# Kernel tuning notes

Measured on AMD Instinct MI355X. Metric: run time of the kernel, lower is better.

Reference implementation:

```python
import jax, jax.numpy as jnp
import numpy as np
from jax import lax

TEMP = 65.0
CLIP_DIST = 0.01
EPS = 1e-6  # torch PairwiseDistance eps (added to the difference) and log eps
NTOKEN, NINP, NHID = 32000, 1024, 1024
SEQ_LEN, BSZ, NSAMPLES = 128, 64, 10


def setup_inputs() -> dict:
    key = jax.random.key(0)
    ks = jax.random.split(key, 7)
    data = jax.random.randint(ks[0], (SEQ_LEN, BSZ), 0, NTOKEN)
    samples = jax.random.randint(ks[1], (NSAMPLES, SEQ_LEN * BSZ), 0, NTOKEN)
    # encoder init_weights: uniform(-0.1, 0.1); RNN weights small to avoid tanh saturation
    emb_W = jax.random.uniform(ks[2], (NTOKEN, NINP), minval=-0.1, maxval=0.1, dtype=jnp.float32)
    W_ih = jax.random.normal(ks[3], (NHID, NINP), dtype=jnp.float32) * 0.03
    b_ih = jax.random.normal(ks[4], (NHID,), dtype=jnp.float32) * 0.01
    W_hh = jax.random.normal(ks[5], (NHID, NHID), dtype=jnp.float32) * 0.03
    b_hh = jax.random.normal(ks[6], (NHID,), dtype=jnp.float32) * 0.01
    return {"data": data, "samples": samples, "emb_W": emb_W,
            "W_ih": W_ih, "b_ih": b_ih, "W_hh": W_hh, "b_hh": b_hh}


def _sq_pdist(x, y):
    # torch PairwiseDistance(p=2).pow(2): ||x - y + eps||^2 (no sqrt needed)
    d = x - y + EPS
    return jnp.sum(d * d, axis=-1)


def reference(data, samples, emb_W, W_ih, b_ih, W_hh, b_hh):
    seq_len, bsz = data.shape
    nhid = W_hh.shape[0]
    emb = emb_W[data]                                  # [S, B, ninp]
    h0 = jnp.zeros((bsz, nhid), dtype=emb_W.dtype)

    def step(h, e):
        h_new = jnp.tanh(e @ W_ih.T + b_ih + h @ W_hh.T + b_hh)
        return h_new, h_new

    _, outs = lax.scan(step, h0, emb)                  # [S, B, H]
    raw = jnp.concatenate([h0[None], outs], axis=0)    # [S+1, B, H]

    # positive term: temp * ||h_t - h_{t+1}||^2, summed, averaged over seq_len
    pos = TEMP * _sq_pdist(raw[:-1], raw[1:])          # [S, B]
    loss = pos.sum() / seq_len

    prev = raw[:-1].reshape(seq_len * bsz, nhid)       # [S*B, H]
    samples_emb = emb_W[samples]                       # [ns, S*B, ninp]
    samples_W = samples_emb @ W_ih.T + b_ih            # [ns, S*B, H]
    hiddens_U = prev @ W_hh.T + b_hh                   # [S*B, H]

    out = jnp.tanh(samples_W + hiddens_U[None])        # [ns, S*B, H]
    dist = _sq_pdist(prev[None], out)                  # [ns, S*B]
    dist = jnp.clip(dist, 0.0, CLIP_DIST)
    n = seq_len * bsz
    sum_of_exp = jnp.sum(jnp.exp(-dist), axis=0) / n   # [S*B]
    loss = loss + jnp.log(sum_of_exp + EPS).sum()
    return loss
```

## Files before the change

### kernel.cpp

```cpp
#include <hip/hip_runtime.h>
#include <hip/hip_bf16.h>
#include <cmath>

typedef __bf16 bf16;
typedef __attribute__((ext_vector_type(8))) __bf16 bf16x8;
typedef __attribute__((ext_vector_type(4))) __bf16 bf16x4;
typedef __attribute__((ext_vector_type(4))) float f32x4;
typedef unsigned long long ull;

#define TEMPC 65.0f
#define EPSC 1e-6f
#define PD_OFF 200000

#define GLD_LDS16(gptr, lptr)                                                             \
    __builtin_amdgcn_global_load_lds(                                                     \
        (const __attribute__((address_space(1))) unsigned int*)(gptr),                    \
        (__attribute__((address_space(3))) unsigned int*)(lptr), 16, 0, 0)

__device__ __forceinline__ bf16x8 ald16(const bf16* p)
{
    union { ull u[2]; bf16x8 v; } c;
    c.u[0] = __hip_atomic_load((const ull*)p,     __ATOMIC_RELAXED, __HIP_MEMORY_SCOPE_AGENT);
    c.u[1] = __hip_atomic_load((const ull*)p + 1, __ATOMIC_RELAXED, __HIP_MEMORY_SCOPE_AGENT);
    return c.v;
}

__global__ void conv2_kernel(const float* __restrict__ a, bf16* __restrict__ ab,
                             const float* __restrict__ b, bf16* __restrict__ bb)
{
    int i = (blockIdx.x * blockDim.x + threadIdx.x) * 4;
    const int stride = gridDim.x * blockDim.x * 4;
    for (; i < 1024 * 1024; i += stride) {
        const float4 va = *(const float4*)(a + i);
        bf16x4 oa; oa[0]=(bf16)va.x; oa[1]=(bf16)va.y; oa[2]=(bf16)va.z; oa[3]=(bf16)va.w;
        *(bf16x4*)(ab + i) = oa;
        const float4 vb = *(const float4*)(b + i);
        bf16x4 ob; ob[0]=(bf16)vb.x; ob[1]=(bf16)vb.y; ob[2]=(bf16)vb.z; ob[3]=(bf16)vb.w;
        *(bf16x4*)(bb + i) = ob;
    }
}

__global__ __launch_bounds__(256, 1)
void fused_kernel(const int* __restrict__ data, const int* __restrict__ samples,
                  const float* __restrict__ embf, const bf16* __restrict__ Wih,
                  const float* __restrict__ bih, bf16* __restrict__ P,
                  bf16* __restrict__ raw, const bf16* __restrict__ Whh,
                  bf16* __restrict__ XWb, const float* __restrict__ bhh,
                  bf16* __restrict__ Ust, int* __restrict__ cnt,
                  float* __restrict__ lacc)
{
    __shared__ __align__(16) char pool[147584];
    const int tid = threadIdx.x;
    const int l   = tid & 63;
    const int w   = tid >> 6;
    const int id  = blockIdx.x;

    if (id < 128) {
        bf16* Wlds = (bf16*)pool;
        char* Hlds = pool + 131072;
        const int group  = id & 7;
        const int slot   = id >> 3;
        const int jbase  = slot * 64;
        const int frow   = l & 15;
        const int kchunk = l >> 4;
        const int jglob  = jbase + w * 16 + frow;
        const int rr     = frow & 7;

        {
            const int jloc = l >> 2;
            const int csw  = ((l & 3) ^ ((l >> 3) & 3)) * 16;
            const char* gsrc = (const char*)Whh + (size_t)(jbase + w * 16 + jloc) * 2048 + csw;
            for (int kk = 0; kk < 32; ++kk)
                GLD_LDS16(gsrc + kk * 64, Wlds + (kk * 4 + w) * 512);
            asm volatile("s_waitcnt vmcnt(0)" ::: "memory");
            __syncthreads();
        }
        const float bh = bhh[jglob];

        const int ksw   = kchunk ^ ((frow >> 1) & 3);
        const bf16* wrd = Wlds + w * 512 + frow * 32 + ksw * 8;
        const char* hrd = Hlds + rr * 2064 + kchunk * 16;
        const int jpair = jglob & ~1;
        float posacc = 0.f;

        for (int t = 0; t < 128; ++t) {
            if (t > 0) {
                if (tid < 4)
                    while (__hip_atomic_load(&cnt[((t * 8 + group) * 4 + tid) * 32],
                                             __ATOMIC_RELAXED, __HIP_MEMORY_SCOPE_AGENT) < 4)
                        __builtin_amdgcn_s_sleep(1);
                __syncthreads();
            }
            const ull* hsrc8 = (const ull*)(raw + (size_t)t * 65536 + group * 8192);
            ull hv[8];
            #pragma unroll
            for (int i = 0; i < 8; ++i)
                hv[i] = __hip_atomic_load(hsrc8 + tid + i * 256,
                                          __ATOMIC_RELAXED, __HIP_MEMORY_SCOPE_AGENT);
            unsigned int xww[4];
            #pragma unroll
            for (int r = 0; r < 4; ++r) {
                const int bc = (kchunk * 4 + r) & 7;
                const size_t row = (size_t)(t * 64 + group * 8 + bc);
                xww[r] = __hip_atomic_load((const unsigned int*)(XWb + row * 1024 + jpair),
                                           __ATOMIC_RELAXED, __HIP_MEMORY_SCOPE_AGENT);
            }
            #pragma unroll
            for (int i = 0; i < 8; ++i)
                *(ull*)(Hlds + i * 2064 + tid * 8) = hv[i];
            __syncthreads();

            f32x4 acc0 = {0.f,0.f,0.f,0.f}, acc1 = {0.f,0.f,0.f,0.f};
            #pragma unroll
            for (int kk = 0; kk < 32; kk += 2) {
                bf16x8 a0 = *(const bf16x8*)(hrd + kk * 64);
                bf16x8 a1 = *(const bf16x8*)(hrd + kk * 64 + 64);
                acc0 = __builtin_amdgcn_mfma_f32_16x16x32_bf16(a0, *(const bf16x8*)(wrd + kk * 2048),       acc0, 0, 0, 0);
                acc1 = __builtin_amdgcn_mfma_f32_16x16x32_bf16(a1, *(const bf16x8*)(wrd + (kk + 1) * 2048), acc1, 0, 0, 0);
            }

            for (;;) {
                bool bad = false;
                #pragma unroll
                for (int r = 0; r < 4; ++r) bad |= (xww[r] == 0xFFFFFFFFu);
                if (!bad) break;
                #pragma unroll
                for (int r = 0; r < 4; ++r)
                    if (xww[r] == 0xFFFFFFFFu) {
                        const int bc = (kchunk * 4 + r) & 7;
                        const size_t row = (size_t)(t * 64 + group * 8 + bc);
                        xww[r] = __hip_atomic_load((const unsigned int*)(XWb + row * 1024 + jpair),
                                                   __ATOMIC_RELAXED, __HIP_MEMORY_SCOPE_AGENT);
                    }
            }

            bf16* rawN = raw + (size_t)(t + 1) * 65536;
            if (l < 32) {
                #pragma unroll
                for (int r = 0; r < 4; ++r) {
                    const int b = (l >> 4) * 4 + r;
                    const unsigned short x16 = (jglob & 1) ? (unsigned short)(xww[r] >> 16)
                                                           : (unsigned short)(xww[r] & 0xFFFF);
                    const float xwv = __builtin_bit_cast(float, (unsigned int)x16 << 16);
                    const float V = acc0[r] + acc1[r] + bh;
                    const float h = tanhf(xwv + V);
                    const size_t row = (size_t)(t * 64 + group * 8 + b);
                    const bf16 ub = (bf16)V;
                    const bf16 hb = (bf16)h;
                    const float ht = (float)*(const bf16*)(Hlds + b * 2064 + jglob * 2);
                    const float pd = ht - (float)hb + EPSC;
                    posacc += pd * pd;
                    unsigned short us = __builtin_bit_cast(unsigned short, ub);
                    unsigned short hs = __builtin_bit_cast(unsigned short, hb);
                    unsigned short un = (unsigned short)__shfl_down((int)us, 1, 64);
                    unsigned short hn = (unsigned short)__shfl_down((int)hs, 1, 64);
                    if ((frow & 1) == 0) {
                        unsigned int up = (unsigned int)us | ((unsigned int)un << 16);
                        unsigned int hp = (unsigned int)hs | ((unsigned int)hn << 16);
                        __hip_atomic_store((unsigned int*)(Ust + row * 1024 + jglob), up,
                                           __ATOMIC_RELAXED, __HIP_MEMORY_SCOPE_AGENT);
                        __hip_atomic_store((unsigned int*)(rawN + (size_t)(group * 8 + b) * 1024 + jglob), hp,
                                           __ATOMIC_RELAXED, __HIP_MEMORY_SCOPE_AGENT);
                    }
                }
            }
            __syncthreads();
            if (tid == 0)
                __hip_atomic_fetch_add(&cnt[(((t + 1) * 8 + group) * 4 + (slot & 3)) * 32], 1,
                                       __ATOMIC_RELAXED, __HIP_MEMORY_SCOPE_AGENT);
        }
        #pragma unroll
        for (int off2 = 32; off2 > 0; off2 >>= 1) posacc += __shfl_down(posacc, off2, 64);
        if (l == 0) atomicAdd(lacc, posacc * (TEMPC / 128.f));
    } else if (id < 2640) {
        bf16* As = (bf16*)pool;
        bf16* Bs = (bf16*)(pool + 16384);
        const int wr = w >> 1, wc = w & 1;
        const bool isXW = (id < 640);

        int mbase, nbase;
        const int rla = w * 32 + (l >> 2);
        const int g8  = ((l & 3) ^ ((l >> 3) & 3)) * 8;
        const float *Af0, *Af1;
        if (isXW) {
            const int q = id - 128;
            mbase = (q >> 3) * 128;
            nbase = (q & 7) * 128;
            Af0 = embf + (size_t)data[mbase + rla] * 1024 + g8;
            Af1 = embf + (size_t)data[mbase + rla + 16] * 1024 + g8;
        } else {
            const int q  = id - 640;
            const int wg = (q & 7) * 250 + (q >> 3);
            mbase = (wg >> 3) * 128;
            nbase = (wg & 7) * 128;
            Af0 = embf + (size_t)(mbase + rla) * 1024 + g8;
            Af1 = embf + (size_t)(mbase + rla + 16) * 1024 + g8;
        }
        const int csw = ((l & 3) ^ ((l >> 3) & 3)) * 16;
        const char* Bsrc0 = (const char*)Wih + (size_t)(nbase + rla) * 2048 + csw;
        const char* Bsrc1 = (const char*)Wih + (size_t)(nbase + rla + 16) * 2048 + csw;
        char* Adst = (char*)As + w * 2048 + l * 16;

        float4 fa00, fa01, fa10, fa11;
        auto issueA = [&](int k) {
            const float* s0 = Af0 + k * 32;
            const float* s1 = Af1 + k * 32;
            fa00 = *(const float4*)s0;  fa01 = *(const float4*)(s0 + 4);
            fa10 = *(const float4*)s1;  fa11 = *(const float4*)(s1 + 4);
        };
        auto writeA = [&](int buf) {
            bf16x8 o0, o1;
            o0[0]=(bf16)fa00.x; o0[1]=(bf16)fa00.y; o0[2]=(bf16)fa00.z; o0[3]=(bf16)fa00.w;
            o0[4]=(bf16)fa01.x; o0[5]=(bf16)fa01.y; o0[6]=(bf16)fa01.z; o0[7]=(bf16)fa01.w;
            o1[0]=(bf16)fa10.x; o1[1]=(bf16)fa10.y; o1[2]=(bf16)fa10.z; o1[3]=(bf16)fa10.w;
            o1[4]=(bf16)fa11.x; o1[5]=(bf16)fa11.y; o1[6]=(bf16)fa11.z; o1[7]=(bf16)fa11.w;
            *(bf16x8*)(Adst + buf * 8192) = o0;
            *(bf16x8*)(Adst + buf * 8192 + 1024) = o1;
        };
        auto stageB = [&](int buf, int kb) {
            bf16* Bs_ = Bs + buf * 4096 + w * 1024;
            GLD_LDS16(Bsrc0 + kb, Bs_);
            GLD_LDS16(Bsrc1 + kb, Bs_ + 512);
        };

        const int frow  = l & 15;
        const int koffE = ((l >> 4) ^ ((frow >> 1) & 3)) * 8;
        const bf16* Ard = As + (wr * 64 + frow) * 32 + koffE;
        const bf16* Brd = Bs + (wc * 64 + frow) * 32 + koffE;

        issueA(0);
        stageB(0, 0);
        writeA(0);
        __syncthreads();

        f32x4 acc[4][4] = {};
        for (int k = 0; k < 32; ++k) {
            if (k + 1 < 32) { issueA(k + 1); stageB((k + 1) & 1, (k + 1) * 64); }
            const bf16* Ab = Ard + (k & 1) * 4096;
            const bf16* Bb = Brd + (k & 1) * 4096;
            bf16x8 af[4], bfr[4];
            #pragma unroll
            for (int mt = 0; mt < 4; ++mt) af[mt]  = *(const bf16x8*)(Ab + mt * 16 * 32);
            #pragma unroll
            for (int nt = 0; nt < 4; ++nt) bfr[nt] = *(const bf16x8*)(Bb + nt * 16 * 32);
            #pragma unroll
            for (int mt = 0; mt < 4; ++mt)
                #pragma unroll
                for (int nt = 0; nt < 4; ++nt)
                    acc[mt][nt] = __builtin_amdgcn_mfma_f32_16x16x32_bf16(af[mt], bfr[nt], acc[mt][nt], 0, 0, 0);
            if (k + 1 < 32) writeA((k + 1) & 1);
            __syncthreads();
        }

        #pragma unroll
        for (int mt = 0; mt < 4; ++mt)
            #pragma unroll
            for (int nt = 0; nt < 4; ++nt) {
                const int colg = nbase + wc * 64 + nt * 16 + frow;
                const float bi = bih[colg];
                #pragma unroll
                for (int r = 0; r < 4; ++r) {
                    const int rowg = mbase + wr * 64 + mt * 16 + (l >> 4) * 4 + r;
                    const bf16 vb = (bf16)(acc[mt][nt][r] + bi);
                    unsigned short vs = __builtin_bit_cast(unsigned short, vb);
                    unsigned short vn = (unsigned short)__shfl_down((int)vs, 1, 64);
                    if ((frow & 1) == 0) {
                        unsigned int pack = (unsigned int)vs | ((unsigned int)vn << 16);
                        bf16* dstbuf = isXW ? XWb : P;
                        __hip_atomic_store((unsigned int*)(dstbuf + (size_t)rowg * 1024 + colg),
                                           pack, __ATOMIC_RELAXED, __HIP_MEMORY_SCOPE_AGENT);
                    }
                }
            }
        if (!isXW) {
            __syncthreads();
            if (tid == 0)
                __hip_atomic_fetch_add(&cnt[PD_OFF], 1,
                                       __ATOMIC_RELAXED, __HIP_MEMORY_SCOPE_AGENT);
        }
    } else {
        const int n  = id - 2640;
        const int r0 = n * 16;
        const int t  = r0 >> 6;
        const int g0 = (r0 & 63) >> 3;
        if (tid < 8) {
            const int g   = g0 + (tid >> 2);
            const int sub = tid & 3;
            while (__hip_atomic_load(&cnt[(((t + 1) * 8 + g) * 4 + sub) * 32],
                                     __ATOMIC_RELAXED, __HIP_MEMORY_SCOPE_AGENT) < 4)
                __builtin_amdgcn_s_sleep(8);
        } else if (tid == 8) {
            while (__hip_atomic_load(&cnt[PD_OFF],
                                     __ATOMIC_RELAXED, __HIP_MEMORY_SCOPE_AGENT) < 2000)
                __builtin_amdgcn_s_sleep(8);
        }
        __syncthreads();

        for (int i = 0; i < 4; ++i) {
            const int r = r0 + w * 4 + i;
            const bf16* u  = Ust + (size_t)r * 1024;
            const bf16* pv = raw + (size_t)r * 1024;
            float uf[16], vf[16];
            {
                bf16x8 u0 = ald16(u + l * 8);
                bf16x8 u1 = ald16(u + 512 + l * 8);
                bf16x8 v0 = ald16(pv + l * 8);
                bf16x8 v1 = ald16(pv + 512 + l * 8);
                #pragma unroll
                for (int j = 0; j < 8; ++j) {
                    uf[j] = (float)u0[j]; uf[8 + j] = (float)u1[j];
                    vf[j] = (float)v0[j]; vf[8 + j] = (float)v1[j];
                }
            }
            float se = 0.f;
            #pragma unroll
            for (int s = 0; s < 10; ++s) {
                const int tok = samples[s * 8192 + r];
                const bf16* pr = P + (size_t)tok * 1024;
                bf16x8 p0 = ald16(pr + l * 8);
                bf16x8 p1 = ald16(pr + 512 + l * 8);
                float d2 = 0.f;
                #pragma unroll
                for (int j = 0; j < 8; ++j) {
                    const float o0 = tanhf((float)p0[j] + uf[j]);
                    const float d0 = vf[j] - o0 + EPSC;
                    d2 += d0 * d0;
                    const float o1 = tanhf((float)p1[j] + uf[8 + j]);
                    const float d1 = vf[8 + j] - o1 + EPSC;
                    d2 += d1 * d1;
                }
                #pragma unroll
                for (int off = 1; off < 64; off <<= 1)
                    d2 += __shfl_xor(d2, off, 64);
                se += expf(-fminf(d2, 0.01f));
            }
            if (l == 0) atomicAdd(lacc, logf(se * (1.f / 8192.f) + EPSC));
        }
    }
}

__global__ void fin_kernel(const float* __restrict__ lacc, float* __restrict__ out)
{
    if (threadIdx.x == 0) out[0] = lacc[0];
}

extern "C" void kernel_launch(void* const* d_in, const int* in_sizes, int n_in,
                              void* d_out, int out_size, void* d_ws, size_t ws_size,
                              hipStream_t stream)
{
    const int*   data    = (const int*)d_in[0];
    const int*   samples = (const int*)d_in[1];
    const float* emb     = (const float*)d_in[2];
    const float* Wih     = (const float*)d_in[3];
    const float* bih     = (const float*)d_in[4];
    const float* Whh     = (const float*)d_in[5];
    const float* bhh     = (const float*)d_in[6];

    char* ws = (char*)d_ws;
    size_t off = 0;
    auto alloc = [&](size_t bytes) { void* p = ws + off; off += (bytes + 255) & ~(size_t)255; return p; };
    bf16*  Wih_b = (bf16*)alloc((size_t)1024 * 1024 * 2);
    bf16*  Whh_b = (bf16*)alloc((size_t)1024 * 1024 * 2);
    bf16*  P     = (bf16*)alloc((size_t)32000 * 1024 * 2);
    bf16*  XWb   = (bf16*)alloc((size_t)8192 * 1024 * 2);
    bf16*  Ust   = (bf16*)alloc((size_t)8192 * 1024 * 2);
    bf16*  raw   = (bf16*)alloc((size_t)129 * 64 * 1024 * 2);
    float* lacc  = (float*)alloc(256);
    int*   cnt   = (int*)alloc(1048576);

    hipMemsetAsync(raw, 0, 64 * 1024 * 2, stream);
    hipMemsetAsync(XWb, 0xFF, (size_t)8192 * 1024 * 2, stream);
    hipMemsetAsync(lacc, 0, 256, stream);
    hipMemsetAsync(cnt,  0, 1048576, stream);

    conv2_kernel<<<512, 256, 0, stream>>>(Wih, Wih_b, Whh, Whh_b);

    fused_kernel<<<3152, 256, 0, stream>>>(data, samples, emb, Wih_b, bih, P,
                                           raw, Whh_b, XWb, bhh, Ust, cnt, lacc);

    fin_kernel<<<1, 64, 0, stream>>>(lacc, (float*)d_out);
}
```

Baseline: 615.3 us.

## Pre-convert embedding table to bf16 and pipeline GEMM A loads via direct-to-LDS

A separate conversion kernel now turns the whole 32000x1024 embedding table into bf16, so the GEMM blocks can stage both A and B tiles with global_load_lds. The main loop moves to a two-stage prefetch with explicit vmcnt waits and raw barriers instead of register-staged fp32 loads plus converts. The tail loss blocks are also split finer, one row per wave and 4 rows per block, raising the grid to 4688 blocks. The trade-off is an extra pass that reads 128MB and writes 64MB up front, in exchange for halving the GEMM A-side traffic and removing VGPR conversion from the inner loop.

```diff
diff --git a/kernel.cpp b/kernel.cpp
--- a/kernel.cpp
+++ b/kernel.cpp
@@ -25,24 +25,32 @@
     return c.v;
 }
 
-__global__ void conv2_kernel(const float* __restrict__ a, bf16* __restrict__ ab,
+__global__ void conv3_kernel(const float* __restrict__ e, bf16* __restrict__ eb,
+                             const float* __restrict__ a, bf16* __restrict__ ab,
                              const float* __restrict__ b, bf16* __restrict__ bb)
 {
-    int i = (blockIdx.x * blockDim.x + threadIdx.x) * 4;
+    const int base   = (blockIdx.x * blockDim.x + threadIdx.x) * 4;
     const int stride = gridDim.x * blockDim.x * 4;
-    for (; i < 1024 * 1024; i += stride) {
-        const float4 va = *(const float4*)(a + i);
-        bf16x4 oa; oa[0]=(bf16)va.x; oa[1]=(bf16)va.y; oa[2]=(bf16)va.z; oa[3]=(bf16)va.w;
-        *(bf16x4*)(ab + i) = oa;
-        const float4 vb = *(const float4*)(b + i);
-        bf16x4 ob; ob[0]=(bf16)vb.x; ob[1]=(bf16)vb.y; ob[2]=(bf16)vb.z; ob[3]=(bf16)vb.w;
-        *(bf16x4*)(bb + i) = ob;
+    for (int i = base; i < 32000 * 1024; i += stride) {
+        const float4 v = *(const float4*)(e + i);
+        bf16x4 o; o[0]=(bf16)v.x; o[1]=(bf16)v.y; o[2]=(bf16)v.z; o[3]=(bf16)v.w;
+        *(bf16x4*)(eb + i) = o;
+    }
+    for (int i = base; i < 1024 * 1024; i += stride) {
+        const float4 v = *(const float4*)(a + i);
+        bf16x4 o; o[0]=(bf16)v.x; o[1]=(bf16)v.y; o[2]=(bf16)v.z; o[3]=(bf16)v.w;
+        *(bf16x4*)(ab + i) = o;
+    }
+    for (int i = base; i < 1024 * 1024; i += stride) {
+        const float4 v = *(const float4*)(b + i);
+        bf16x4 o; o[0]=(bf16)v.x; o[1]=(bf16)v.y; o[2]=(bf16)v.z; o[3]=(bf16)v.w;
+        *(bf16x4*)(bb + i) = o;
     }
 }
 
 __global__ __launch_bounds__(256, 1)
 void fused_kernel(const int* __restrict__ data, const int* __restrict__ samples,
-                  const float* __restrict__ embf, const bf16* __restrict__ Wih,
+                  const bf16* __restrict__ emb, const bf16* __restrict__ Wih,
                   const float* __restrict__ bih, bf16* __restrict__ P,
                   bf16* __restrict__ raw, const bf16* __restrict__ Whh,
                   bf16* __restrict__ XWb, const float* __restrict__ bhh,
@@ -179,63 +187,48 @@
         const bool isXW = (id < 640);
 
         int mbase, nbase;
-        const int rla = w * 32 + (l >> 2);
-        const int g8  = ((l & 3) ^ ((l >> 3) & 3)) * 8;
-        const float *Af0, *Af1;
+        const char *Asrc0, *Asrc1;
+        const int r0 = w * 32 + (l >> 2);
+        const int csw = ((l & 3) ^ ((l >> 3) & 3)) * 16;
         if (isXW) {
             const int q = id - 128;
             mbase = (q >> 3) * 128;
             nbase = (q & 7) * 128;
-            Af0 = embf + (size_t)data[mbase + rla] * 1024 + g8;
-            Af1 = embf + (size_t)data[mbase + rla + 16] * 1024 + g8;
+            Asrc0 = (const char*)emb + (size_t)data[mbase + r0] * 2048 + csw;
+            Asrc1 = (const char*)emb + (size_t)data[mbase + r0 + 16] * 2048 + csw;
         } else {
             const int q  = id - 640;
             const int wg = (q & 7) * 250 + (q >> 3);
             mbase = (wg >> 3) * 128;
             nbase = (wg & 7) * 128;
-            Af0 = embf + (size_t)(mbase + rla) * 1024 + g8;
-            Af1 = embf + (size_t)(mbase + rla + 16) * 1024 + g8;
-        }
-        const int csw = ((l & 3) ^ ((l >> 3) & 3)) * 16;
-        const char* Bsrc0 = (const char*)Wih + (size_t)(nbase + rla) * 2048 + csw;
-        const char* Bsrc1 = (const char*)Wih + (size_t)(nbase + rla + 16) * 2048 + csw;
-        char* Adst = (char*)As + w * 2048 + l * 16;
-
-        float4 fa00, fa01, fa10, fa11;
-        auto issueA = [&](int k) {
-            const float* s0 = Af0 + k * 32;
-            const float* s1 = Af1 + k * 32;
-            fa00 = *(const float4*)s0;  fa01 = *(const float4*)(s0 + 4);
-            fa10 = *(const float4*)s1;  fa11 = *(const float4*)(s1 + 4);
-        };
-        auto writeA = [&](int buf) {
-            bf16x8 o0, o1;
-            o0[0]=(bf16)fa00.x; o0[1]=(bf16)fa00.y; o0[2]=(bf16)fa00.z; o0[3]=(bf16)fa00.w;
-            o0[4]=(bf16)fa01.x; o0[5]=(bf16)fa01.y; o0[6]=(bf16)fa01.z; o0[7]=(bf16)fa01.w;
-            o1[0]=(bf16)fa10.x; o1[1]=(bf16)fa10.y; o1[2]=(bf16)fa10.z; o1[3]=(bf16)fa10.w;
-            o1[4]=(bf16)fa11.x; o1[5]=(bf16)fa11.y; o1[6]=(bf16)fa11.z; o1[7]=(bf16)fa11.w;
-            *(bf16x8*)(Adst + buf * 8192) = o0;
-            *(bf16x8*)(Adst + buf * 8192 + 1024) = o1;
-        };
-        auto stageB = [&](int buf, int kb) {
+            Asrc0 = (const char*)emb + (size_t)(mbase + r0) * 2048 + csw;
+            Asrc1 = (const char*)emb + (size_t)(mbase + r0 + 16) * 2048 + csw;
+        }
+        const char* Bsrc0 = (const char*)Wih + (size_t)(nbase + r0) * 2048 + csw;
+        const char* Bsrc1 = (const char*)Wih + (size_t)(nbase + r0 + 16) * 2048 + csw;
+
+        const int frow  = l & 15;
+        const int koffE = (((l >> 4) ^ ((frow >> 1) & 3)) * 8);
+        const bf16* Ard = As + (wr * 64 + frow) * 32 + koffE;
+        const bf16* Brd = Bs + (wc * 64 + frow) * 32 + koffE;
+
+        auto stage = [&](int buf, int kb) {
+            bf16* As_ = As + buf * 4096 + w * 1024;
             bf16* Bs_ = Bs + buf * 4096 + w * 1024;
+            GLD_LDS16(Asrc0 + kb, As_);
+            GLD_LDS16(Asrc1 + kb, As_ + 512);
             GLD_LDS16(Bsrc0 + kb, Bs_);
             GLD_LDS16(Bsrc1 + kb, Bs_ + 512);
         };
 
-        const int frow  = l & 15;
-        const int koffE = ((l >> 4) ^ ((frow >> 1) & 3)) * 8;
-        const bf16* Ard = As + (wr * 64 + frow) * 32 + koffE;
-        const bf16* Brd = Bs + (wc * 64 + frow) * 32 + koffE;
-
-        issueA(0);
-        stageB(0, 0);
-        writeA(0);
-        __syncthreads();
+        stage(0, 0);
+        stage(1, 64);
 
         f32x4 acc[4][4] = {};
         for (int k = 0; k < 32; ++k) {
-            if (k + 1 < 32) { issueA(k + 1); stageB((k + 1) & 1, (k + 1) * 64); }
+            if (k == 31) asm volatile("s_waitcnt vmcnt(0)" ::: "memory");
+            else         asm volatile("s_waitcnt vmcnt(4)" ::: "memory");
+            __builtin_amdgcn_s_barrier();
             const bf16* Ab = Ard + (k & 1) * 4096;
             const bf16* Bb = Brd + (k & 1) * 4096;
             bf16x8 af[4], bfr[4];
@@ -248,10 +241,12 @@
                 #pragma unroll
                 for (int nt = 0; nt < 4; ++nt)
                     acc[mt][nt] = __builtin_amdgcn_mfma_f32_16x16x32_bf16(af[mt], bfr[nt], acc[mt][nt], 0, 0, 0);
-            if (k + 1 < 32) writeA((k + 1) & 1);
-            __syncthreads();
-        }
-
+            asm volatile("s_waitcnt lgkmcnt(0)" ::: "memory");
+            __builtin_amdgcn_s_barrier();
+            if (k + 2 < 32) stage(k & 1, (k + 2) * 64);
+        }
+
+        bf16* dstbuf = isXW ? XWb : P;
         #pragma unroll
         for (int mt = 0; mt < 4; ++mt)
             #pragma unroll
@@ -266,7 +261,6 @@
                     unsigned short vn = (unsigned short)__shfl_down((int)vs, 1, 64);
                     if ((frow & 1) == 0) {
                         unsigned int pack = (unsigned int)vs | ((unsigned int)vn << 16);
-                        bf16* dstbuf = isXW ? XWb : P;
                         __hip_atomic_store((unsigned int*)(dstbuf + (size_t)rowg * 1024 + colg),
                                            pack, __ATOMIC_RELAXED, __HIP_MEMORY_SCOPE_AGENT);
                     }
@@ -280,62 +274,58 @@
         }
     } else {
         const int n  = id - 2640;
-        const int r0 = n * 16;
+        const int r0 = n * 4;
         const int t  = r0 >> 6;
-        const int g0 = (r0 & 63) >> 3;
-        if (tid < 8) {
-            const int g   = g0 + (tid >> 2);
-            const int sub = tid & 3;
-            while (__hip_atomic_load(&cnt[(((t + 1) * 8 + g) * 4 + sub) * 32],
+        const int g  = (r0 & 63) >> 3;
+        if (tid < 4) {
+            while (__hip_atomic_load(&cnt[(((t + 1) * 8 + g) * 4 + tid) * 32],
                                      __ATOMIC_RELAXED, __HIP_MEMORY_SCOPE_AGENT) < 4)
                 __builtin_amdgcn_s_sleep(8);
-        } else if (tid == 8) {
+        } else if (tid == 4) {
             while (__hip_atomic_load(&cnt[PD_OFF],
                                      __ATOMIC_RELAXED, __HIP_MEMORY_SCOPE_AGENT) < 2000)
                 __builtin_amdgcn_s_sleep(8);
         }
         __syncthreads();
 
-        for (int i = 0; i < 4; ++i) {
-            const int r = r0 + w * 4 + i;
-            const bf16* u  = Ust + (size_t)r * 1024;
-            const bf16* pv = raw + (size_t)r * 1024;
-            float uf[16], vf[16];
-            {
-                bf16x8 u0 = ald16(u + l * 8);
-                bf16x8 u1 = ald16(u + 512 + l * 8);
-                bf16x8 v0 = ald16(pv + l * 8);
-                bf16x8 v1 = ald16(pv + 512 + l * 8);
-                #pragma unroll
-                for (int j = 0; j < 8; ++j) {
-                    uf[j] = (float)u0[j]; uf[8 + j] = (float)u1[j];
-                    vf[j] = (float)v0[j]; vf[8 + j] = (float)v1[j];
-                }
-            }
-            float se = 0.f;
-            #pragma unroll
-            for (int s = 0; s < 10; ++s) {
-                const int tok = samples[s * 8192 + r];
-                const bf16* pr = P + (size_t)tok * 1024;
-                bf16x8 p0 = ald16(pr + l * 8);
-                bf16x8 p1 = ald16(pr + 512 + l * 8);
-                float d2 = 0.f;
-                #pragma unroll
-                for (int j = 0; j < 8; ++j) {
-                    const float o0 = tanhf((float)p0[j] + uf[j]);
-                    const float d0 = vf[j] - o0 + EPSC;
-                    d2 += d0 * d0;
-                    const float o1 = tanhf((float)p1[j] + uf[8 + j]);
-                    const float d1 = vf[8 + j] - o1 + EPSC;
-                    d2 += d1 * d1;
-                }
-                #pragma unroll
-                for (int off = 1; off < 64; off <<= 1)
-                    d2 += __shfl_xor(d2, off, 64);
-                se += expf(-fminf(d2, 0.01f));
-            }
-            if (l == 0) atomicAdd(lacc, logf(se * (1.f / 8192.f) + EPSC));
-        }
+        const int r = r0 + w;
+        const bf16* u  = Ust + (size_t)r * 1024;
+        const bf16* pv = raw + (size_t)r * 1024;
+        float uf[16], vf[16];
+        {
+            bf16x8 u0 = ald16(u + l * 8);
+            bf16x8 u1 = ald16(u + 512 + l * 8);
+            bf16x8 v0 = ald16(pv + l * 8);
+            bf16x8 v1 = ald16(pv + 512 + l * 8);
+            #pragma unroll
+            for (int j = 0; j < 8; ++j) {
+                uf[j] = (float)u0[j]; uf[8 + j] = (float)u1[j];
+                vf[j] = (float)v0[j]; vf[8 + j] = (float)v1[j];
+            }
+        }
+        float se = 0.f;
+        #pragma unroll
+        for (int s = 0; s < 10; ++s) {
+            const int tok = samples[s * 8192 + r];
+            const bf16* pr = P + (size_t)tok * 1024;
+            bf16x8 p0 = ald16(pr + l * 8);
+            bf16x8 p1 = ald16(pr + 512 + l * 8);
+            float d2 = 0.f;
+            #pragma unroll
+            for (int j = 0; j < 8; ++j) {
+                const float o0 = tanhf((float)p0[j] + uf[j]);
+                const float d0 = vf[j] - o0 + EPSC;
+                d2 += d0 * d0;
+                const float o1 = tanhf((float)p1[j] + uf[8 + j]);
+                const float d1 = vf[8 + j] - o1 + EPSC;
+                d2 += d1 * d1;
+            }
+            #pragma unroll
+            for (int off = 1; off < 64; off <<= 1)
+                d2 += __shfl_xor(d2, off, 64);
+            se += expf(-fminf(d2, 0.01f));
+        }
+        if (l == 0) atomicAdd(lacc, logf(se * (1.f / 8192.f) + EPSC));
     }
 }
 
@@ -359,6 +349,7 @@
     char* ws = (char*)d_ws;
     size_t off = 0;
     auto alloc = [&](size_t bytes) { void* p = ws + off; off += (bytes + 255) & ~(size_t)255; return p; };
+    bf16*  emb_b = (bf16*)alloc((size_t)32000 * 1024 * 2);
     bf16*  Wih_b = (bf16*)alloc((size_t)1024 * 1024 * 2);
     bf16*  Whh_b = (bf16*)alloc((size_t)1024 * 1024 * 2);
     bf16*  P     = (bf16*)alloc((size_t)32000 * 1024 * 2);
@@ -373,9 +364,9 @@
     hipMemsetAsync(lacc, 0, 256, stream);
     hipMemsetAsync(cnt,  0, 1048576, stream);
 
-    conv2_kernel<<<512, 256, 0, stream>>>(Wih, Wih_b, Whh, Whh_b);
-
-    fused_kernel<<<3152, 256, 0, stream>>>(data, samples, emb, Wih_b, bih, P,
+    conv3_kernel<<<2048, 256, 0, stream>>>(emb, emb_b, Wih, Wih_b, Whh, Whh_b);
+
+    fused_kernel<<<4688, 256, 0, stream>>>(data, samples, emb_b, Wih_b, bih, P,
                                            raw, Whh_b, XWb, bhh, Ust, cnt, lacc);
 
     fin_kernel<<<1, 64, 0, stream>>>(lacc, (float*)d_out);
```

New measurement: 590.4 us. 1.04x faster.
